# Kernel tuning notes

Measured on AMD Instinct MI355X. Metric: run time of the kernel, lower is better.

The kernel has to match this reference:

```python
import jax, jax.numpy as jnp
import numpy as np

N, L, D = 256, 512, 512


def _attention(x, W_in, W_out, apply_tanh):
    # x: [N, L, D]; 'general' attention: project query, score against context (=x)
    q = jnp.einsum('bld,ed->ble', x, W_in)          # [N, L, D]
    scores = jnp.einsum('bld,bmd->blm', q, x)       # [N, L, L]
    w = jax.nn.softmax(scores, axis=-1)             # softmax over keys
    mix = jnp.einsum('blm,bmd->bld', w, x)          # [N, L, D]
    comb = jnp.concatenate([mix, q], axis=-1)       # [N, L, 2D]
    out = jnp.einsum('blc,dc->bld', comb, W_out)    # Linear(2D, D), no bias
    return jnp.tanh(out) if apply_tanh else out


def setup_inputs() -> dict:
    key = jax.random.key(0)
    k1, k2, k3, k4, k5 = jax.random.split(key, 5)
    s = 0.02
    return {
        'embeddings': jax.random.normal(k1, (N, L, D), dtype=jnp.float32),
        'W_in1': jax.random.normal(k2, (D, D), dtype=jnp.float32) * s,
        'W_out1': jax.random.normal(k3, (D, 2 * D), dtype=jnp.float32) * s,
        'W_in2': jax.random.normal(k4, (D, D), dtype=jnp.float32) * s,
        'W_out2': jax.random.normal(k5, (D, 2 * D), dtype=jnp.float32) * s,
    }


def reference(embeddings, W_in1, W_out1, W_in2, W_out2):
    x = _attention(embeddings, W_in1, W_out1, apply_tanh=True)   # block 1 (tanh)
    x = _attention(x, W_in2, W_out2, apply_tanh=False)           # block 2 (no tanh)
    # transpose(1,2) + avg_pool1d over full length == mean over L
    pooled = jnp.mean(x, axis=1)                                  # [N, D]
    return pooled.reshape(pooled.shape[0], -1, 1, 1)              # [N, D, 1, 1]
```

## Files before the change

kernel.cpp:

```cpp
#include <hip/hip_runtime.h>
#include <cstdint>
#include <cstddef>

typedef uint16_t u16;
typedef __attribute__((ext_vector_type(8))) short bf16x8;
typedef __attribute__((ext_vector_type(4))) float f32x4;
typedef __attribute__((ext_vector_type(4))) uint16_t u16x4;

#define GLOBAL_AS(p) (const __attribute__((address_space(1))) void*)(p)
#define LDS_AS(p)    (__attribute__((address_space(3))) void*)(p)

__device__ __forceinline__ u16 f2b(float f){
  uint32_t u = __float_as_uint(f);
  u += 0x7fff + ((u >> 16) & 1);
  return (u16)(u >> 16);
}
__device__ __forceinline__ float b2f(u16 h){
  return __uint_as_float(((uint32_t)h) << 16);
}

__global__ void cvt_bf16_kernel(const float* __restrict__ src, u16* __restrict__ dst, int n){
  int i = (blockIdx.x * 256 + threadIdx.x) * 4;
  if (i >= n) return;
  float4 f = *(const float4*)(src + i);
  u16x4 o; o.x = f2b(f.x); o.y = f2b(f.y); o.z = f2b(f.z); o.w = f2b(f.w);
  *(u16x4*)(dst + i) = o;
}

__global__ void cvtT_kernel(const float* __restrict__ src, u16* __restrict__ x, u16* __restrict__ xT){
  __shared__ u16 tile[64][68];
  size_t b = blockIdx.y;
  int t = blockIdx.x;
  int r0 = (t >> 3) * 64, c0 = (t & 7) * 64;
  const float* s = src + b * 262144;
  u16* dx = x + b * 262144;
  u16* dT = xT + b * 262144;
  int tx = threadIdx.x & 63, ty = threadIdx.x >> 6;
  #pragma unroll
  for (int k = 0; k < 16; k++){
    int r = ty * 16 + k;
    u16 v = f2b(s[(size_t)(r0 + r) * 512 + c0 + tx]);
    dx[(size_t)(r0 + r) * 512 + c0 + tx] = v;
    tile[r][tx] = v;
  }
  __syncthreads();
  #pragma unroll
  for (int k = 0; k < 16; k++){
    int c = ty * 16 + k;
    dT[(size_t)(c0 + c) * 512 + r0 + tx] = tile[tx][c];
  }
}

__global__ void transpose512_kernel(const u16* __restrict__ src, u16* __restrict__ dst){
  __shared__ u16 tile[64][68];
  size_t b = blockIdx.y;
  int t = blockIdx.x;
  int r0 = (t >> 3) * 64, c0 = (t & 7) * 64;
  const u16* s = src + b * 262144;
  u16* d = dst + b * 262144;
  int tx = threadIdx.x & 63, ty = threadIdx.x >> 6;
  #pragma unroll
  for (int k = 0; k < 16; k++){
    int r = ty * 16 + k;
    tile[r][tx] = s[(size_t)(r0 + r) * 512 + c0 + tx];
  }
  __syncthreads();
  #pragma unroll
  for (int k = 0; k < 16; k++){
    int c = ty * 16 + k;
    d[(size_t)(c0 + c) * 512 + r0 + tx] = tile[tx][c];
  }
}

__global__ __launch_bounds__(256, 1) void attn_kernel(
    const u16* __restrict__ q, const u16* __restrict__ x, const u16* __restrict__ xT,
    u16* __restrict__ mix)
{
  __shared__ __align__(16) u16 U[64 * 520];
  __shared__ __align__(16) u16 Bx[512 * 32];
  __shared__ float stats[2][64][4];
  const int64_t E = 262144;
  int64_t bat = blockIdx.y;
  q += bat * E; x += bat * E; xT += bat * E; mix += bat * E;
  int m0 = blockIdx.x * 64;
  int tid = threadIdx.x, lane = tid & 63, w = tid >> 6;
  int fr = lane & 15, qd = lane >> 4, fq = qd * 8;

  #pragma unroll
  for (int c = 0; c < 16; c++){
    int id = c * 256 + tid;
    int row = id >> 6, cb = id & 63;
    *(bf16x8*)&U[row * 520 + cb * 8] =
        *(const bf16x8*)(q + (size_t)(m0 + row) * 512 + cb * 8);
  }

  f32x4 acc[4][8];
  #pragma unroll
  for (int i = 0; i < 4; i++)
    #pragma unroll
    for (int j = 0; j < 8; j++) acc[i][j] = (f32x4){0.f, 0.f, 0.f, 0.f};

  for (int k0 = 0; k0 < 512; k0 += 32){
    #pragma unroll
    for (int s = 0; s < 8; s++){
      const u16* g = x + (size_t)(s * 64 + (tid >> 2)) * 512 + k0 + (tid & 3) * 8;
      __builtin_amdgcn_global_load_lds(GLOBAL_AS(g), LDS_AS(&Bx[s * 2048 + tid * 8]), 16, 0, 0);
    }
    __syncthreads();
    bf16x8 af[4], bfr[8];
    #pragma unroll
    for (int i = 0; i < 4; i++) af[i]  = *(const bf16x8*)&U[(i * 16 + fr) * 520 + k0 + fq];
    #pragma unroll
    for (int j = 0; j < 8; j++) bfr[j] = *(const bf16x8*)&Bx[(w * 128 + j * 16 + fr) * 32 + fq];
    #pragma unroll
    for (int i = 0; i < 4; i++)
      #pragma unroll
      for (int j = 0; j < 8; j++)
        acc[i][j] = __builtin_amdgcn_mfma_f32_16x16x32_bf16(af[i], bfr[j], acc[i][j], 0, 0, 0);
    __syncthreads();
  }

  float mfull[4][4], inv[4][4];
  #pragma unroll
  for (int i = 0; i < 4; i++)
    #pragma unroll
    for (int r = 0; r < 4; r++){
      float m = acc[i][0][r];
      #pragma unroll
      for (int j = 1; j < 8; j++) m = fmaxf(m, acc[i][j][r]);
      #pragma unroll
      for (int o = 1; o <= 8; o <<= 1) m = fmaxf(m, __shfl_xor(m, o));
      mfull[i][r] = m;
    }
  if (fr == 0){
    #pragma unroll
    for (int i = 0; i < 4; i++)
      #pragma unroll
      for (int r = 0; r < 4; r++) stats[0][i * 16 + qd * 4 + r][w] = mfull[i][r];
  }
  __syncthreads();
  #pragma unroll
  for (int i = 0; i < 4; i++)
    #pragma unroll
    for (int r = 0; r < 4; r++){
      int row = i * 16 + qd * 4 + r;
      float m = fmaxf(fmaxf(stats[0][row][0], stats[0][row][1]),
                      fmaxf(stats[0][row][2], stats[0][row][3]));
      mfull[i][r] = m;
      float s = 0.f;
      #pragma unroll
      for (int j = 0; j < 8; j++){
        float e = __expf(acc[i][j][r] - m);
        acc[i][j][r] = e; s += e;
      }
      #pragma unroll
      for (int o = 1; o <= 8; o <<= 1) s += __shfl_xor(s, o);
      inv[i][r] = s;
    }
  if (fr == 0){
    #pragma unroll
    for (int i = 0; i < 4; i++)
      #pragma unroll
      for (int r = 0; r < 4; r++) stats[1][i * 16 + qd * 4 + r][w] = inv[i][r];
  }
  __syncthreads();
  #pragma unroll
  for (int i = 0; i < 4; i++)
    #pragma unroll
    for (int r = 0; r < 4; r++){
      int row = i * 16 + qd * 4 + r;
      inv[i][r] = 1.0f / (stats[1][row][0] + stats[1][row][1] +
                          stats[1][row][2] + stats[1][row][3]);
    }
  #pragma unroll
  for (int i = 0; i < 4; i++)
    #pragma unroll
    for (int r = 0; r < 4; r++)
      #pragma unroll
      for (int j = 0; j < 8; j++){
        int row = i * 16 + qd * 4 + r;
        int col = w * 128 + j * 16 + fr;
        uint32_t mine = f2b(acc[i][j][r] * inv[i][r]);
        uint32_t oth = (uint32_t)__shfl_xor((int)mine, 1);
        if (!(fr & 1)) *(uint32_t*)&U[row * 520 + col] = mine | (oth << 16);
      }
  __syncthreads();

  #pragma unroll
  for (int i = 0; i < 4; i++)
    #pragma unroll
    for (int j = 0; j < 8; j++) acc[i][j] = (f32x4){0.f, 0.f, 0.f, 0.f};
  for (int k0 = 0; k0 < 512; k0 += 32){
    #pragma unroll
    for (int s = 0; s < 8; s++){
      const u16* g = xT + (size_t)(s * 64 + (tid >> 2)) * 512 + k0 + (tid & 3) * 8;
      __builtin_amdgcn_global_load_lds(GLOBAL_AS(g), LDS_AS(&Bx[s * 2048 + tid * 8]), 16, 0, 0);
    }
    __syncthreads();
    bf16x8 af[4], bfr[8];
    #pragma unroll
    for (int i = 0; i < 4; i++) af[i]  = *(const bf16x8*)&U[(i * 16 + fr) * 520 + k0 + fq];
    #pragma unroll
    for (int j = 0; j < 8; j++) bfr[j] = *(const bf16x8*)&Bx[(w * 128 + j * 16 + fr) * 32 + fq];
    #pragma unroll
    for (int i = 0; i < 4; i++)
      #pragma unroll
      for (int j = 0; j < 8; j++)
        acc[i][j] = __builtin_amdgcn_mfma_f32_16x16x32_bf16(af[i], bfr[j], acc[i][j], 0, 0, 0);
    __syncthreads();
  }
  #pragma unroll
  for (int i = 0; i < 4; i++)
    #pragma unroll
    for (int j = 0; j < 8; j++)
      #pragma unroll
      for (int r = 0; r < 4; r++)
        mix[(size_t)(m0 + i * 16 + qd * 4 + r) * 512 + w * 128 + j * 16 + fr] =
            f2b(acc[i][j][r]);
}

template<bool SPLIT, bool TANH, bool POOL, typename CT>
__global__ __launch_bounds__(256, 2) void gemm_bt_kernel(
    const u16* __restrict__ A0, const u16* __restrict__ A1,
    const u16* __restrict__ B, CT* __restrict__ C,
    int K, int ldb, int64_t aBatch, int64_t bBatch, int64_t cBatch,
    float* __restrict__ poolOut, int b0)
{
  __shared__ __align__(16) u16 As[128 * 32];
  __shared__ __align__(16) u16 Bs[128 * 32];
  int64_t bat = blockIdx.y;
  int m0 = (blockIdx.x & 3) * 128, n0 = (blockIdx.x >> 2) * 128;
  A0 += bat * aBatch;
  if (SPLIT) A1 += bat * aBatch;
  B += bat * bBatch;
  if (!POOL) C += bat * cBatch;
  int tid = threadIdx.x, lane = tid & 63;
  int w = tid >> 6;
  int wm = (w >> 1) * 64, wn = (w & 1) * 64;
  f32x4 acc[4][4];
  #pragma unroll
  for (int i = 0; i < 4; i++)
    #pragma unroll
    for (int j = 0; j < 4; j++) acc[i][j] = (f32x4){0.f, 0.f, 0.f, 0.f};

  int sRow = tid >> 2, sCol = (tid & 3) * 8;
  int fr = lane & 15, fq = (lane >> 4) * 8;

  for (int k0 = 0; k0 < K; k0 += 32){
    const u16* Ap = A0; int kk = k0;
    if (SPLIT && k0 >= 512){ Ap = A1; kk = k0 - 512; }
    const u16* ga = Ap + (size_t)(m0 + sRow) * 512 + kk + sCol;
    const u16* gb = B  + (size_t)(n0 + sRow) * ldb + k0 + sCol;
    __builtin_amdgcn_global_load_lds(GLOBAL_AS(ga),                    LDS_AS(&As[tid * 8]),        16, 0, 0);
    __builtin_amdgcn_global_load_lds(GLOBAL_AS(ga + (size_t)64 * 512), LDS_AS(&As[2048 + tid * 8]), 16, 0, 0);
    __builtin_amdgcn_global_load_lds(GLOBAL_AS(gb),                    LDS_AS(&Bs[tid * 8]),        16, 0, 0);
    __builtin_amdgcn_global_load_lds(GLOBAL_AS(gb + (size_t)64 * ldb), LDS_AS(&Bs[2048 + tid * 8]), 16, 0, 0);
    __syncthreads();
    bf16x8 af[4], bfr[4];
    #pragma unroll
    for (int i = 0; i < 4; i++) af[i]  = *(const bf16x8*)&As[(wm + i * 16 + fr) * 32 + fq];
    #pragma unroll
    for (int j = 0; j < 4; j++) bfr[j] = *(const bf16x8*)&Bs[(wn + j * 16 + fr) * 32 + fq];
    #pragma unroll
    for (int i = 0; i < 4; i++)
      #pragma unroll
      for (int j = 0; j < 4; j++)
        acc[i][j] = __builtin_amdgcn_mfma_f32_16x16x32_bf16(af[i], bfr[j], acc[i][j], 0, 0, 0);
    __syncthreads();
  }

  if constexpr (POOL){
    #pragma unroll
    for (int j = 0; j < 4; j++){
      float p = 0.f;
      #pragma unroll
      for (int i = 0; i < 4; i++)
        #pragma unroll
        for (int r = 0; r < 4; r++) p += acc[i][j][r];
      p += __shfl_xor(p, 16);
      p += __shfl_xor(p, 32);
      if (lane < 16){
        int col = n0 + wn + j * 16 + lane;
        atomicAdd(poolOut + ((size_t)(b0) + bat) * 512 + col, p * (1.0f / 512.0f));
      }
    }
  } else {
    int cq = (lane >> 4) * 4, cc = lane & 15;
    #pragma unroll
    for (int i = 0; i < 4; i++){
      #pragma unroll
      for (int j = 0; j < 4; j++){
        #pragma unroll
        for (int r = 0; r < 4; r++){
          int row = m0 + wm + i * 16 + cq + r;
          int col = n0 + wn + j * 16 + cc;
          float v = acc[i][j][r];
          if (TANH) v = tanhf(v);
          if constexpr (sizeof(CT) == 4) C[(size_t)row * 512 + col] = v;
          else                           C[(size_t)row * 512 + col] = f2b(v);
        }
      }
    }
  }
}

extern "C" void kernel_launch(void* const* d_in, const int* in_sizes, int n_in,
                              void* d_out, int out_size, void* d_ws, size_t ws_size,
                              hipStream_t stream) {
  const float* emb   = (const float*)d_in[0];
  const float* Win1  = (const float*)d_in[1];
  const float* Wout1 = (const float*)d_in[2];
  const float* Win2  = (const float*)d_in[3];
  const float* Wout2 = (const float*)d_in[4];
  float* out = (float*)d_out;

  int CB = 256;
  while (CB > 1 && (4ull << 20) + (size_t)CB * (5ull * 524288ull) > ws_size) CB >>= 1;
  const int64_t E = 262144;

  char* wsb = (char*)d_ws;
  u16* Win1b  = (u16*)wsb;
  u16* Wout1b = Win1b + 262144;
  u16* Win2b  = Wout1b + 524288;
  u16* Wout2b = Win2b + 262144;
  u16* base = (u16*)(wsb + (4 << 20));
  u16* Ar = base;
  u16* Br = base + (size_t)CB * E;
  u16* Cr = base + 2 * (size_t)CB * E;
  u16* Dr = base + 3 * (size_t)CB * E;
  u16* Fr = base + 4 * (size_t)CB * E;

  hipMemsetAsync(d_out, 0, (size_t)out_size * sizeof(float), stream);

  cvt_bf16_kernel<<<256, 256, 0, stream>>>(Win1,  Win1b,  262144);
  cvt_bf16_kernel<<<512, 256, 0, stream>>>(Wout1, Wout1b, 524288);
  cvt_bf16_kernel<<<256, 256, 0, stream>>>(Win2,  Win2b,  262144);
  cvt_bf16_kernel<<<512, 256, 0, stream>>>(Wout2, Wout2b, 524288);

  dim3 gg(16, CB);
  dim3 ga(8, CB);
  dim3 gt(64, CB);

  for (int c = 0; c < 256 / CB; c++){
    const float* embc = emb + (size_t)c * CB * 262144;
    int b0 = c * CB;

    cvtT_kernel<<<gt, 256, 0, stream>>>(embc, Ar, Cr);
    gemm_bt_kernel<false,false,false,u16><<<gg, 256, 0, stream>>>(
        Ar, nullptr, Win1b, Br, 512, 512, E, 0, E, nullptr, 0);
    attn_kernel<<<ga, 256, 0, stream>>>(Br, Ar, Cr, Fr);
    gemm_bt_kernel<true,true,false,u16><<<gg, 256, 0, stream>>>(
        Fr, Br, Wout1b, Dr, 1024, 1024, E, 0, E, nullptr, 0);

    transpose512_kernel<<<gt, 256, 0, stream>>>(Dr, Cr);
    gemm_bt_kernel<false,false,false,u16><<<gg, 256, 0, stream>>>(
        Dr, nullptr, Win2b, Ar, 512, 512, E, 0, E, nullptr, 0);
    attn_kernel<<<ga, 256, 0, stream>>>(Ar, Dr, Cr, Fr);
    gemm_bt_kernel<true,false,true,u16><<<gg, 256, 0, stream>>>(
        Fr, Ar, Wout2b, (u16*)nullptr, 1024, 1024, E, 0, 0, out, b0);
  }
}
```

Measured before the change: 1.967 ms.

## Widen attention block to 512 threads and remap blocks for XCD-local batches

The attention kernel now runs 8 waves per block instead of 4, each holding a 64x64 score slice rather than 64x128. This halves per-thread accumulators and allows two blocks per CU. The grid is flattened and block ids are remapped so that all 8 query tiles of one batch land on the same XCD, which should improve L2 reuse of x and xT. The cost is a cross-wave softmax reduction over 8 partials and a minimum chunk batch of 8.

After: 1.851 ms. 1.06x faster.

```diff
diff --git a/kernel.cpp b/kernel.cpp
--- a/kernel.cpp
+++ b/kernel.cpp
@@ -72,114 +72,106 @@
   }
 }
 
-__global__ __launch_bounds__(256, 1) void attn_kernel(
+__global__ __launch_bounds__(512, 2) void attn_kernel(
     const u16* __restrict__ q, const u16* __restrict__ x, const u16* __restrict__ xT,
-    u16* __restrict__ mix)
+    u16* __restrict__ mix, int batPerXcd)
 {
   __shared__ __align__(16) u16 U[64 * 520];
   __shared__ __align__(16) u16 Bx[512 * 32];
-  __shared__ float stats[2][64][4];
+  __shared__ float stats[2][64][8];
   const int64_t E = 262144;
-  int64_t bat = blockIdx.y;
+  int id = blockIdx.x;
+  int tile = (id >> 3) & 7;
+  int64_t bat = (int64_t)(id & 7) * batPerXcd + (id >> 6);
   q += bat * E; x += bat * E; xT += bat * E; mix += bat * E;
-  int m0 = blockIdx.x * 64;
+  int m0 = tile * 64;
   int tid = threadIdx.x, lane = tid & 63, w = tid >> 6;
   int fr = lane & 15, qd = lane >> 4, fq = qd * 8;
 
   #pragma unroll
-  for (int c = 0; c < 16; c++){
-    int id = c * 256 + tid;
-    int row = id >> 6, cb = id & 63;
+  for (int c = 0; c < 8; c++){
+    int id2 = c * 512 + tid;
+    int row = id2 >> 6, cb = id2 & 63;
     *(bf16x8*)&U[row * 520 + cb * 8] =
         *(const bf16x8*)(q + (size_t)(m0 + row) * 512 + cb * 8);
   }
 
-  f32x4 acc[4][8];
-  #pragma unroll
-  for (int i = 0; i < 4; i++)
-    #pragma unroll
-    for (int j = 0; j < 8; j++) acc[i][j] = (f32x4){0.f, 0.f, 0.f, 0.f};
+  f32x4 acc[4][4];
+  #pragma unroll
+  for (int i = 0; i < 4; i++)
+    #pragma unroll
+    for (int j = 0; j < 4; j++) acc[i][j] = (f32x4){0.f, 0.f, 0.f, 0.f};
 
   for (int k0 = 0; k0 < 512; k0 += 32){
     #pragma unroll
-    for (int s = 0; s < 8; s++){
-      const u16* g = x + (size_t)(s * 64 + (tid >> 2)) * 512 + k0 + (tid & 3) * 8;
-      __builtin_amdgcn_global_load_lds(GLOBAL_AS(g), LDS_AS(&Bx[s * 2048 + tid * 8]), 16, 0, 0);
-    }
-    __syncthreads();
-    bf16x8 af[4], bfr[8];
+    for (int s = 0; s < 4; s++){
+      const u16* g = x + (size_t)(s * 128 + (tid >> 2)) * 512 + k0 + (tid & 3) * 8;
+      __builtin_amdgcn_global_load_lds(GLOBAL_AS(g), LDS_AS(&Bx[s * 4096 + tid * 8]), 16, 0, 0);
+    }
+    __syncthreads();
+    bf16x8 af[4], bfr[4];
     #pragma unroll
     for (int i = 0; i < 4; i++) af[i]  = *(const bf16x8*)&U[(i * 16 + fr) * 520 + k0 + fq];
     #pragma unroll
-    for (int j = 0; j < 8; j++) bfr[j] = *(const bf16x8*)&Bx[(w * 128 + j * 16 + fr) * 32 + fq];
+    for (int j = 0; j < 4; j++) bfr[j] = *(const bf16x8*)&Bx[(w * 64 + j * 16 + fr) * 32 + fq];
     #pragma unroll
     for (int i = 0; i < 4; i++)
       #pragma unroll
-      for (int j = 0; j < 8; j++)
+      for (int j = 0; j < 4; j++)
         acc[i][j] = __builtin_amdgcn_mfma_f32_16x16x32_bf16(af[i], bfr[j], acc[i][j], 0, 0, 0);
     __syncthreads();
   }
 
-  float mfull[4][4], inv[4][4];
+  float inv[4][4];
   #pragma unroll
   for (int i = 0; i < 4; i++)
     #pragma unroll
     for (int r = 0; r < 4; r++){
       float m = acc[i][0][r];
       #pragma unroll
-      for (int j = 1; j < 8; j++) m = fmaxf(m, acc[i][j][r]);
+      for (int j = 1; j < 4; j++) m = fmaxf(m, acc[i][j][r]);
       #pragma unroll
       for (int o = 1; o <= 8; o <<= 1) m = fmaxf(m, __shfl_xor(m, o));
-      mfull[i][r] = m;
-    }
-  if (fr == 0){
-    #pragma unroll
-    for (int i = 0; i < 4; i++)
-      #pragma unroll
-      for (int r = 0; r < 4; r++) stats[0][i * 16 + qd * 4 + r][w] = mfull[i][r];
-  }
+      if (fr == 0) stats[0][i * 16 + qd * 4 + r][w] = m;
+    }
   __syncthreads();
   #pragma unroll
   for (int i = 0; i < 4; i++)
     #pragma unroll
     for (int r = 0; r < 4; r++){
       int row = i * 16 + qd * 4 + r;
-      float m = fmaxf(fmaxf(stats[0][row][0], stats[0][row][1]),
-                      fmaxf(stats[0][row][2], stats[0][row][3]));
-      mfull[i][r] = m;
+      float m = stats[0][row][0];
+      #pragma unroll
+      for (int t = 1; t < 8; t++) m = fmaxf(m, stats[0][row][t]);
       float s = 0.f;
       #pragma unroll
-      for (int j = 0; j < 8; j++){
+      for (int j = 0; j < 4; j++){
         float e = __expf(acc[i][j][r] - m);
         acc[i][j][r] = e; s += e;
       }
       #pragma unroll
       for (int o = 1; o <= 8; o <<= 1) s += __shfl_xor(s, o);
-      inv[i][r] = s;
-    }
-  if (fr == 0){
-    #pragma unroll
-    for (int i = 0; i < 4; i++)
-      #pragma unroll
-      for (int r = 0; r < 4; r++) stats[1][i * 16 + qd * 4 + r][w] = inv[i][r];
-  }
+      if (fr == 0) stats[1][row][w] = s;
+    }
   __syncthreads();
   #pragma unroll
   for (int i = 0; i < 4; i++)
     #pragma unroll
     for (int r = 0; r < 4; r++){
       int row = i * 16 + qd * 4 + r;
-      inv[i][r] = 1.0f / (stats[1][row][0] + stats[1][row][1] +
-                          stats[1][row][2] + stats[1][row][3]);
+      float s = stats[1][row][0];
+      #pragma unroll
+      for (int t = 1; t < 8; t++) s += stats[1][row][t];
+      inv[i][r] = 1.0f / s;
     }
   #pragma unroll
   for (int i = 0; i < 4; i++)
     #pragma unroll
     for (int r = 0; r < 4; r++)
       #pragma unroll
-      for (int j = 0; j < 8; j++){
+      for (int j = 0; j < 4; j++){
         int row = i * 16 + qd * 4 + r;
-        int col = w * 128 + j * 16 + fr;
+        int col = w * 64 + j * 16 + fr;
         uint32_t mine = f2b(acc[i][j][r] * inv[i][r]);
         uint32_t oth = (uint32_t)__shfl_xor((int)mine, 1);
         if (!(fr & 1)) *(uint32_t*)&U[row * 520 + col] = mine | (oth << 16);
@@ -189,33 +181,33 @@
   #pragma unroll
   for (int i = 0; i < 4; i++)
     #pragma unroll
-    for (int j = 0; j < 8; j++) acc[i][j] = (f32x4){0.f, 0.f, 0.f, 0.f};
+    for (int j = 0; j < 4; j++) acc[i][j] = (f32x4){0.f, 0.f, 0.f, 0.f};
   for (int k0 = 0; k0 < 512; k0 += 32){
     #pragma unroll
-    for (int s = 0; s < 8; s++){
-      const u16* g = xT + (size_t)(s * 64 + (tid >> 2)) * 512 + k0 + (tid & 3) * 8;
-      __builtin_amdgcn_global_load_lds(GLOBAL_AS(g), LDS_AS(&Bx[s * 2048 + tid * 8]), 16, 0, 0);
-    }
-    __syncthreads();
-    bf16x8 af[4], bfr[8];
+    for (int s = 0; s < 4; s++){
+      const u16* g = xT + (size_t)(s * 128 + (tid >> 2)) * 512 + k0 + (tid & 3) * 8;
+      __builtin_amdgcn_global_load_lds(GLOBAL_AS(g), LDS_AS(&Bx[s * 4096 + tid * 8]), 16, 0, 0);
+    }
+    __syncthreads();
+    bf16x8 af[4], bfr[4];
     #pragma unroll
     for (int i = 0; i < 4; i++) af[i]  = *(const bf16x8*)&U[(i * 16 + fr) * 520 + k0 + fq];
     #pragma unroll
-    for (int j = 0; j < 8; j++) bfr[j] = *(const bf16x8*)&Bx[(w * 128 + j * 16 + fr) * 32 + fq];
+    for (int j = 0; j < 4; j++) bfr[j] = *(const bf16x8*)&Bx[(w * 64 + j * 16 + fr) * 32 + fq];
     #pragma unroll
     for (int i = 0; i < 4; i++)
       #pragma unroll
-      for (int j = 0; j < 8; j++)
+      for (int j = 0; j < 4; j++)
         acc[i][j] = __builtin_amdgcn_mfma_f32_16x16x32_bf16(af[i], bfr[j], acc[i][j], 0, 0, 0);
     __syncthreads();
   }
   #pragma unroll
   for (int i = 0; i < 4; i++)
     #pragma unroll
-    for (int j = 0; j < 8; j++)
+    for (int j = 0; j < 4; j++)
       #pragma unroll
       for (int r = 0; r < 4; r++)
-        mix[(size_t)(m0 + i * 16 + qd * 4 + r) * 512 + w * 128 + j * 16 + fr] =
+        mix[(size_t)(m0 + i * 16 + qd * 4 + r) * 512 + w * 64 + j * 16 + fr] =
             f2b(acc[i][j][r]);
 }
 
@@ -315,7 +307,7 @@
   float* out = (float*)d_out;
 
   int CB = 256;
-  while (CB > 1 && (4ull << 20) + (size_t)CB * (5ull * 524288ull) > ws_size) CB >>= 1;
+  while (CB > 8 && (4ull << 20) + (size_t)CB * (5ull * 524288ull) > ws_size) CB >>= 1;
   const int64_t E = 262144;
 
   char* wsb = (char*)d_ws;
@@ -338,8 +330,9 @@
   cvt_bf16_kernel<<<512, 256, 0, stream>>>(Wout2, Wout2b, 524288);
 
   dim3 gg(16, CB);
-  dim3 ga(8, CB);
   dim3 gt(64, CB);
+  int nAttnBlocks = CB * 8;
+  int batPerXcd = CB / 8;
 
   for (int c = 0; c < 256 / CB; c++){
     const float* embc = emb + (size_t)c * CB * 262144;
@@ -348,14 +341,14 @@
     cvtT_kernel<<<gt, 256, 0, stream>>>(embc, Ar, Cr);
     gemm_bt_kernel<false,false,false,u16><<<gg, 256, 0, stream>>>(
         Ar, nullptr, Win1b, Br, 512, 512, E, 0, E, nullptr, 0);
-    attn_kernel<<<ga, 256, 0, stream>>>(Br, Ar, Cr, Fr);
+    attn_kernel<<<nAttnBlocks, 512, 0, stream>>>(Br, Ar, Cr, Fr, batPerXcd);
     gemm_bt_kernel<true,true,false,u16><<<gg, 256, 0, stream>>>(
         Fr, Br, Wout1b, Dr, 1024, 1024, E, 0, E, nullptr, 0);
 
     transpose512_kernel<<<gt, 256, 0, stream>>>(Dr, Cr);
     gemm_bt_kernel<false,false,false,u16><<<gg, 256, 0, stream>>>(
         Dr, nullptr, Win2b, Ar, 512, 512, E, 0, E, nullptr, 0);
-    attn_kernel<<<ga, 256, 0, stream>>>(Ar, Dr, Cr, Fr);
+    attn_kernel<<<nAttnBlocks, 512, 0, stream>>>(Ar, Dr, Cr, Fr, batPerXcd);
     gemm_bt_kernel<true,false,true,u16><<<gg, 256, 0, stream>>>(
         Fr, Ar, Wout2b, (u16*)nullptr, 1024, 1024, E, 0, 0, out, b0);
   }
```
